# Performance work log

Measured on AMD Instinct MI355X. Metric: run time of the kernel, lower is better.

Reference implementation:

```python
import jax
import jax.numpy as jnp
import numpy as np
from jax import lax

NEG = jnp.float32(-1e30)  # safe 'log zero' (avoids NaNs in logaddexp grads)
EPS = 1e-7                # Keras ctc_batch_cost epsilon


def setup_inputs() -> dict:
    key = jax.random.key(0)
    k1, k2, k3 = jax.random.split(key, 3)
    B, T, C, L = 256, 512, 128, 64
    logits = jax.random.normal(k1, (B, T, C), dtype=jnp.float32)
    y_pred = jax.nn.softmax(logits, axis=-1)  # layer receives softmax probs
    labels = jax.random.randint(k2, (B, L), 0, C - 1)  # blank (C-1) excluded
    label_length = jax.random.randint(k3, (B, 1), 16, L + 1).astype(jnp.int32)
    input_length = jnp.full((B, 1), T, dtype=jnp.int32)
    return {"y_pred": y_pred, "labels": labels,
            "input_length": input_length, "label_length": label_length}


def _ctc_loss(y_pred, labels, input_length, label_length):
    B, T, C = y_pred.shape
    L = labels.shape[1]
    S = 2 * L + 1            # extended label: blank,l1,blank,l2,...,blank
    blank = C - 1            # Keras/TF ctc_batch_cost uses last class as blank

    logp = jnp.log(y_pred + EPS)                       # [B,T,C]
    s = jnp.arange(S)
    lab_idx = jnp.clip(s // 2, 0, L - 1)               # safe index for even s
    lab_ext = jnp.where(s % 2 == 1, labels[:, lab_idx], blank)  # [B,S]

    # log-probs of extended-label symbols at every time step: [B,T,S]
    lp = jnp.take_along_axis(
        logp, jnp.broadcast_to(lab_ext[:, None, :], (B, T, S)), axis=2)
    lpT = jnp.transpose(lp, (1, 0, 2))                 # [T,B,S]

    # skip transition s-2 -> s allowed iff label at s is not blank and differs
    # from label at s-2
    lab_m2 = jnp.pad(lab_ext, ((0, 0), (2, 0)), constant_values=-1)[:, :S]
    skip = (lab_ext != blank) & (lab_ext != lab_m2) & (s[None, :] >= 2)

    alpha0 = jnp.where(s[None, :] < 2, lpT[0], NEG)    # start at s=0 or s=1

    def step(alpha, lp_row):
        a1 = alpha
        a2 = jnp.pad(alpha, ((0, 0), (1, 0)), constant_values=NEG)[:, :S]
        a3 = jnp.pad(alpha, ((0, 0), (2, 0)), constant_values=NEG)[:, :S]
        a3 = jnp.where(skip, a3, NEG)
        new = jnp.logaddexp(jnp.logaddexp(a1, a2), a3) + lp_row
        return new, new

    _, alphas = lax.scan(step, alpha0, lpT[1:])        # [T-1,B,S]
    alphas = jnp.concatenate([alpha0[None], alphas], axis=0)  # [T,B,S]

    b = jnp.arange(B)
    t_idx = input_length[:, 0].astype(jnp.int32) - 1
    alpha_T = alphas[t_idx, b, :]                      # [B,S] at last valid t
    s_end = 2 * label_length[:, 0].astype(jnp.int32)   # final blank position
    a_last = alpha_T[b, s_end]
    a_prev = alpha_T[b, s_end - 1]
    return -jnp.logaddexp(a_last, a_prev)[:, None]     # [B,1]


def reference(y_pred, labels, input_length, label_length):
    # CTCLossLayer computes ctc_batch_cost and registers it via add_loss;
    # the loss tensor [B,1] is the computation of interest.
    return _ctc_loss(y_pred, labels, input_length, label_length)
```

## Files before the change

### kernel.cpp

```cpp
#include <hip/hip_runtime.h>

#define EPSF  (1e-7f)
#define LN2F  (0.69314718055994530942f)

#if __has_builtin(__builtin_amdgcn_logf)
#define LOG2(x) __builtin_amdgcn_logf(x)
#else
#define LOG2(x) __log2f(x)
#endif

template<int CTRL>
__device__ __forceinline__ int dpp_i(int x) {
    return __builtin_amdgcn_update_dpp(x, x, CTRL, 0xF, 0xF, true);
}

__device__ __forceinline__ float shift_up1_f(float x, bool rowhead) {
    int xi = __float_as_int(x);
    int sh = dpp_i<0x111>(xi);
    int bc = dpp_i<0x142>(xi);
    return __int_as_float(rowhead ? bc : sh);
}
__device__ __forceinline__ int shift_up1_i(int x, bool rowhead) {
    int sh = dpp_i<0x111>(x);
    int bc = dpp_i<0x142>(x);
    return rowhead ? bc : sh;
}

__global__ __launch_bounds__(64, 1)
void ctc_fwd_kernel(const float* __restrict__ y_pred,
                    const int*   __restrict__ labels,
                    const int*   __restrict__ input_length,
                    const int*   __restrict__ label_length,
                    float*       __restrict__ out,
                    int T, int C, int L)
{
    const int b    = blockIdx.x;
    const int lane = threadIdx.x;
    const int Tin  = input_length[b];
    const int ll   = label_length[b];

    const int  l       = labels[(size_t)b * L + lane];
    const int  lprev   = __shfl_up(l, 1);
    const bool skip    = (lane >= 1) && (l != lprev);
    const bool rowhead = ((lane & 15) == 0);
    const bool lane0   = (lane == 0);
    const int  src     = l >> 1;
    const bool comp    = (l & 1) != 0;

    const float2* rowp = (const float2*)(y_pred + (size_t)b * T * C) + lane;
    const int rstride  = C >> 1;

    float2 buf[16];
    float ylA[16], ybA[16];
    float ylB[16], ybB[16];
    float a0 = 0.0f, ao = 0.0f, ae = 0.0f;
    int   esum = 0;
    float fsc  = 1.0f;

    auto prefetch = [&](int t0) {
        #pragma unroll
        for (int j = 0; j < 16; ++j) {
            int t = t0 + j; t = (t < T) ? t : (T - 1);
            buf[j] = rowp[(size_t)t * rstride];
        }
    };
    auto gather = [&](float* yl, float* yb) {
        #pragma unroll
        for (int j = 0; j < 16; ++j) {
            float2 y = buf[j];
            float gx = __shfl(y.x, src);
            float gy = __shfl(y.y, src);
            float gb = __int_as_float(
                __builtin_amdgcn_readlane(__float_as_int(y.y), 63));
            yl[j] = (comp ? gy : gx) + EPSF;
            yb[j] = gb + EPSF;
        }
    };
    auto renorm = [&]() {
        float lm    = fmaxf(ae, ao);
        float basis = (lm > 0.0f) ? lm : a0;
        int   e  = (__float_as_int(basis) >> 23) & 0xFF;
        float sc = __int_as_float((254 - e) << 23);
        ae *= sc; ao *= sc; a0 *= sc;
        esum += e - 127;
        int en = shift_up1_i(esum, rowhead);
        int de = en - esum;
        de = de < -127 ? -127 : (de > 127 ? 127 : de);
        fsc = __int_as_float((127 + de) << 23);
    };
    auto chain = [&](const float* yl, const float* yb, int t0) {
        #pragma unroll
        for (int j = 0; j < 16; ++j) {
            int t = t0 + j;
            if (t < Tin) {
                if (t == 0) {
                    a0 = yb[0];
                    ao = lane0 ? yl[0] : 0.0f;
                    ae = 0.0f;
                } else {
                    float sae = shift_up1_f(ae, rowhead);
                    float sao = shift_up1_f(ao, rowhead);
                    float a2  = lane0 ? a0 : sae * fsc;
                    float a3  = skip ? sao * fsc : 0.0f;
                    float nao = (ao + a2 + a3) * yl[j];
                    float nae = (ae + ao) * yb[j];
                    a0 *= yb[j];
                    ao = nao;
                    ae = nae;
                }
            }
            if ((j & 3) == 3) renorm();
        }
    };

    const int NB = T / 16;
    prefetch(0);
    gather(ylA, ybA);
    prefetch(16);
    for (int kb = 0; kb < NB; kb += 2) {
        if (kb + 1 < NB) gather(ylB, ybB);
        prefetch((kb + 2) * 16);
        chain(ylA, ybA, kb * 16);
        if (kb + 2 < NB) gather(ylA, ybA);
        prefetch((kb + 3) * 16);
        if (kb + 1 < NB) chain(ylB, ybB, (kb + 1) * 16);
    }

    if (lane == ll - 1) {
        float p = ae + ao;
        out[b] = -(LOG2(p) + (float)esum) * LN2F;
    }
}

extern "C" void kernel_launch(void* const* d_in, const int* in_sizes, int n_in,
                              void* d_out, int out_size, void* d_ws, size_t ws_size,
                              hipStream_t stream) {
    const float* y_pred       = (const float*)d_in[0];
    const int*   labels       = (const int*)d_in[1];
    const int*   input_length = (const int*)d_in[2];
    const int*   label_length = (const int*)d_in[3];
    float*       out          = (float*)d_out;

    const int B = in_sizes[2];
    const int L = in_sizes[1] / B;
    const int T = 512;
    const int C = 128;

    ctc_fwd_kernel<<<B, 64, 0, stream>>>(y_pred, labels, input_length,
                                         label_length, out, T, C, L);
}
```

Measured before the change: 129.1 us.

## Gather label probabilities through LDS staging instead of cross-lane shuffles

Each 16-step block of probability rows is written to a double-buffered shared-memory tile, and each lane reads its label's probability with a single LDS load. This replaces two ds_bpermute shuffles plus a select per time step. The pipeline is restructured around two register load buffers and a hardcoded count of 32 blocks, so T=512 and C=128 are now assumed. No barrier is used because the block is a single wavefront.

```diff
diff --git a/kernel.cpp b/kernel.cpp
--- a/kernel.cpp
+++ b/kernel.cpp
@@ -44,37 +44,36 @@
     const bool skip    = (lane >= 1) && (l != lprev);
     const bool rowhead = ((lane & 15) == 0);
     const bool lane0   = (lane == 0);
-    const int  src     = l >> 1;
-    const bool comp    = (l & 1) != 0;
+
+    __shared__ float smem[2][16][128];
 
     const float2* rowp = (const float2*)(y_pred + (size_t)b * T * C) + lane;
-    const int rstride  = C >> 1;
 
-    float2 buf[16];
-    float ylA[16], ybA[16];
-    float ylB[16], ybB[16];
+    float2 bufA[16], bufB[16];
+    float ylA[16], ylB[16], ybA[16], ybB[16];
     float a0 = 0.0f, ao = 0.0f, ae = 0.0f;
     int   esum = 0;
     float fsc  = 1.0f;
 
-    auto prefetch = [&](int t0) {
+    auto loadbuf = [&](float2* buf, int t0) {
         #pragma unroll
         for (int j = 0; j < 16; ++j) {
             int t = t0 + j; t = (t < T) ? t : (T - 1);
-            buf[j] = rowp[(size_t)t * rstride];
+            buf[j] = rowp[(size_t)t * 64];
         }
     };
-    auto gather = [&](float* yl, float* yb) {
+    auto stage = [&](int r, const float2* buf, float* yb) {
         #pragma unroll
         for (int j = 0; j < 16; ++j) {
-            float2 y = buf[j];
-            float gx = __shfl(y.x, src);
-            float gy = __shfl(y.y, src);
-            float gb = __int_as_float(
-                __builtin_amdgcn_readlane(__float_as_int(y.y), 63));
-            yl[j] = (comp ? gy : gx) + EPSF;
-            yb[j] = gb + EPSF;
+            yb[j] = __int_as_float(__builtin_amdgcn_readlane(
+                        __float_as_int(buf[j].y), 63)) + EPSF;
+            *(float2*)&smem[r][j][2 * lane] = buf[j];
         }
+    };
+    auto readyl = [&](int r, float* yl) {
+        #pragma unroll
+        for (int j = 0; j < 16; ++j)
+            yl[j] = smem[r][j][l] + EPSF;
     };
     auto renorm = [&]() {
         float lm    = fmaxf(ae, ao);
@@ -113,17 +112,22 @@
         }
     };
 
-    const int NB = T / 16;
-    prefetch(0);
-    gather(ylA, ybA);
-    prefetch(16);
-    for (int kb = 0; kb < NB; kb += 2) {
-        if (kb + 1 < NB) gather(ylB, ybB);
-        prefetch((kb + 2) * 16);
-        chain(ylA, ybA, kb * 16);
-        if (kb + 2 < NB) gather(ylA, ybA);
-        prefetch((kb + 3) * 16);
-        if (kb + 1 < NB) chain(ylB, ybB, (kb + 1) * 16);
+    loadbuf(bufA, 0);
+    loadbuf(bufB, 16);
+    stage(0, bufA, ybA);
+    loadbuf(bufA, 32);
+    readyl(0, ylA);
+
+    for (int p = 0; p < 32; p += 2) {
+        stage(1, bufB, ybB);
+        loadbuf(bufB, (p + 3) * 16);
+        readyl(1, ylB);
+        chain(ylA, ybA, p * 16);
+
+        stage(0, bufA, ybA);
+        loadbuf(bufA, (p + 4) * 16);
+        readyl(0, ylA);
+        chain(ylB, ybB, (p + 1) * 16);
     }
 
     if (lane == ll - 1) {
```

Measured after the change: 124.9 us. -3.3%, faster.

## Split into producer wave loading via global_load_lds and consumer wave computing CTC chain

Applied to the files above, without the earlier changes.

Adds a second wave per block that streams 16-step phases of y_pred into a 4-deep LDS ring buffer with direct global-to-LDS loads. The compute wave reads the label and blank probabilities from LDS instead of doing register prefetch plus cross-lane shuffles and readlane gathers. The two waves synchronise with a workgroup barrier per phase. The aim is to take load latency and gather overhead off the serial recurrence. The cost is barrier overhead and a ring-reuse safety that depends on the prefetch distance and on waitcnt encoding.

```diff
diff --git a/kernel.cpp b/kernel.cpp
--- a/kernel.cpp
+++ b/kernel.cpp
@@ -26,7 +26,13 @@
     return rowhead ? bc : sh;
 }
 
-__global__ __launch_bounds__(64, 1)
+__device__ __forceinline__ void wg_barrier() {
+    asm volatile("" ::: "memory");
+    __builtin_amdgcn_s_barrier();
+    asm volatile("" ::: "memory");
+}
+
+__global__ __launch_bounds__(128, 1)
 void ctc_fwd_kernel(const float* __restrict__ y_pred,
                     const int*   __restrict__ labels,
                     const int*   __restrict__ input_length,
@@ -35,100 +41,95 @@
                     int T, int C, int L)
 {
     const int b    = blockIdx.x;
-    const int lane = threadIdx.x;
+    const int wave = threadIdx.x >> 6;
+    const int lane = threadIdx.x & 63;
     const int Tin  = input_length[b];
     const int ll   = label_length[b];
 
-    const int  l       = labels[(size_t)b * L + lane];
-    const int  lprev   = __shfl_up(l, 1);
-    const bool skip    = (lane >= 1) && (l != lprev);
-    const bool rowhead = ((lane & 15) == 0);
-    const bool lane0   = (lane == 0);
-    const int  src     = l >> 1;
-    const bool comp    = (l & 1) != 0;
+    __shared__ float smem[4][16][128];
+    const int NP = T / 16;
 
-    const float2* rowp = (const float2*)(y_pred + (size_t)b * T * C) + lane;
-    const int rstride  = C >> 1;
+    if (wave == 1) {
+        const float* g0 = y_pred + (size_t)b * T * C;
+        auto issue_phase = [&](int ph) {
+            int reg = ph & 3;
+            int phc = (ph < NP) ? ph : (NP - 1);
+            const float* g = g0 + (size_t)phc * 16 * 128;
+            float* lp = &smem[reg][0][0];
+            #pragma unroll
+            for (int c = 0; c < 8; ++c) {
+                __builtin_amdgcn_global_load_lds(
+                    (const __attribute__((address_space(1))) void*)(g + c * 256 + lane * 4),
+                    (__attribute__((address_space(3))) void*)(lp + c * 256),
+                    16, 0, 0);
+            }
+        };
+        issue_phase(0);
+        issue_phase(1);
+        for (int p = 0; p < NP; ++p) {
+            issue_phase(p + 2);
+            __builtin_amdgcn_s_waitcnt(0x4F70);
+            wg_barrier();
+        }
+    } else {
+        const int  l       = labels[(size_t)b * L + lane];
+        const int  lprev   = __shfl_up(l, 1);
+        const bool skip    = (lane >= 1) && (l != lprev);
+        const bool rowhead = ((lane & 15) == 0);
+        const bool lane0   = (lane == 0);
 
-    float2 buf[16];
-    float ylA[16], ybA[16];
-    float ylB[16], ybB[16];
-    float a0 = 0.0f, ao = 0.0f, ae = 0.0f;
-    int   esum = 0;
-    float fsc  = 1.0f;
+        float a0 = 0.0f, ao = 0.0f, ae = 0.0f;
+        int   esum = 0;
+        float fsc  = 1.0f;
 
-    auto prefetch = [&](int t0) {
-        #pragma unroll
-        for (int j = 0; j < 16; ++j) {
-            int t = t0 + j; t = (t < T) ? t : (T - 1);
-            buf[j] = rowp[(size_t)t * rstride];
-        }
-    };
-    auto gather = [&](float* yl, float* yb) {
-        #pragma unroll
-        for (int j = 0; j < 16; ++j) {
-            float2 y = buf[j];
-            float gx = __shfl(y.x, src);
-            float gy = __shfl(y.y, src);
-            float gb = __int_as_float(
-                __builtin_amdgcn_readlane(__float_as_int(y.y), 63));
-            yl[j] = (comp ? gy : gx) + EPSF;
-            yb[j] = gb + EPSF;
-        }
-    };
-    auto renorm = [&]() {
-        float lm    = fmaxf(ae, ao);
-        float basis = (lm > 0.0f) ? lm : a0;
-        int   e  = (__float_as_int(basis) >> 23) & 0xFF;
-        float sc = __int_as_float((254 - e) << 23);
-        ae *= sc; ao *= sc; a0 *= sc;
-        esum += e - 127;
-        int en = shift_up1_i(esum, rowhead);
-        int de = en - esum;
-        de = de < -127 ? -127 : (de > 127 ? 127 : de);
-        fsc = __int_as_float((127 + de) << 23);
-    };
-    auto chain = [&](const float* yl, const float* yb, int t0) {
-        #pragma unroll
-        for (int j = 0; j < 16; ++j) {
-            int t = t0 + j;
-            if (t < Tin) {
-                if (t == 0) {
-                    a0 = yb[0];
-                    ao = lane0 ? yl[0] : 0.0f;
-                    ae = 0.0f;
-                } else {
-                    float sae = shift_up1_f(ae, rowhead);
-                    float sao = shift_up1_f(ao, rowhead);
-                    float a2  = lane0 ? a0 : sae * fsc;
-                    float a3  = skip ? sao * fsc : 0.0f;
-                    float nao = (ao + a2 + a3) * yl[j];
-                    float nae = (ae + ao) * yb[j];
-                    a0 *= yb[j];
-                    ao = nao;
-                    ae = nae;
+        for (int p = 0; p < NP; ++p) {
+            wg_barrier();
+            const int reg = p & 3;
+            float ylv[16], ybv[16];
+            #pragma unroll
+            for (int j = 0; j < 16; ++j) {
+                ylv[j] = smem[reg][j][l] + EPSF;
+                ybv[j] = smem[reg][j][127] + EPSF;
+            }
+            #pragma unroll
+            for (int j = 0; j < 16; ++j) {
+                int t = p * 16 + j;
+                if (t < Tin) {
+                    if (t == 0) {
+                        a0 = ybv[0];
+                        ao = lane0 ? ylv[0] : 0.0f;
+                        ae = 0.0f;
+                    } else {
+                        float sae = shift_up1_f(ae, rowhead);
+                        float sao = shift_up1_f(ao, rowhead);
+                        float a2  = lane0 ? a0 : sae * fsc;
+                        float a3  = skip ? sao * fsc : 0.0f;
+                        float nao = (ao + a2 + a3) * ylv[j];
+                        float nae = (ae + ao) * ybv[j];
+                        a0 *= ybv[j];
+                        ao = nao;
+                        ae = nae;
+                    }
+                }
+                if ((j & 3) == 3) {
+                    float lm    = fmaxf(ae, ao);
+                    float basis = (lm > 0.0f) ? lm : a0;
+                    int   e  = (__float_as_int(basis) >> 23) & 0xFF;
+                    float sc = __int_as_float((254 - e) << 23);
+                    ae *= sc; ao *= sc; a0 *= sc;
+                    esum += e - 127;
+                    int en = shift_up1_i(esum, rowhead);
+                    int de = en - esum;
+                    de = de < -127 ? -127 : (de > 127 ? 127 : de);
+                    fsc = __int_as_float((127 + de) << 23);
                 }
             }
-            if ((j & 3) == 3) renorm();
         }
-    };
 
-    const int NB = T / 16;
-    prefetch(0);
-    gather(ylA, ybA);
-    prefetch(16);
-    for (int kb = 0; kb < NB; kb += 2) {
-        if (kb + 1 < NB) gather(ylB, ybB);
-        prefetch((kb + 2) * 16);
-        chain(ylA, ybA, kb * 16);
-        if (kb + 2 < NB) gather(ylA, ybA);
-        prefetch((kb + 3) * 16);
-        if (kb + 1 < NB) chain(ylB, ybB, (kb + 1) * 16);
-    }
-
-    if (lane == ll - 1) {
-        float p = ae + ao;
-        out[b] = -(LOG2(p) + (float)esum) * LN2F;
+        if (lane == ll - 1) {
+            float pfin = ae + ao;
+            out[b] = -(LOG2(pfin) + (float)esum) * LN2F;
+        }
     }
 }
 
@@ -146,6 +147,6 @@
     const int T = 512;
     const int C = 128;
 
-    ctc_fwd_kernel<<<B, 64, 0, stream>>>(y_pred, labels, input_length,
-                                         label_length, out, T, C, L);
+    ctc_fwd_kernel<<<B, 128, 0, stream>>>(y_pred, labels, input_length,
+                                          label_length, out, T, C, L);
 }
```

After: 114.9 us. -11.0%, faster.
